# Kernel tuning notes

Hardware: AMD Instinct MI355X
Metric: run time of the kernel (lower is better)

## Reference

```python
import jax, jax.numpy as jnp
import numpy as np

B, N = 16, 286
EMB_DIM = 4
CLOUD_DIM = 4
NB = 3          # number_of_basis
HID = 150       # radial MLP hidden width
RADIUS = 3.0    # neighbor radius / max_radius of cosine basis
FF = 512


def sp5(x):
    # torch Softplus(beta=5)
    return jax.nn.softplus(5.0 * x) / 5.0


def cosine_basis(r):
    # e3nn CosineBasisModel embedding: cos^2 bumps on [0, RADIUS]
    centers = jnp.linspace(0.0, RADIUS, NB)
    step = centers[1] - centers[0]
    d = (r[..., None] - centers) / step                     # [B,N,N,NB]
    return jnp.cos(jnp.pi / 2 * d) ** 2 * (jnp.abs(d) < 1.0)


def cloud_conv(feats, dist, mask, ws, bs, dim_out):
    # radial MLP on pairwise distances -> per-pair [dim_out, dim_in] kernel (l=0 only)
    x = cosine_basis(dist)
    for w, b in zip(ws[:-1], bs[:-1]):
        x = sp5(x @ w + b)
    R = x @ ws[-1] + bs[-1]                                 # [B,N,N,dim_out*dim_in]
    b_, n_ = dist.shape[0], dist.shape[1]
    k = R.reshape(b_, n_, n_, dim_out, -1) * mask[..., None, None]
    nb = jnp.maximum(mask.sum(-1), 1.0)                     # neighbors per atom [B,N]
    out = jnp.einsum('zabij,zbj->zai', k, feats) / jnp.sqrt(nb)[..., None]
    return out


def setup_inputs() -> dict:
    key = jax.random.key(0)
    ks = jax.random.split(key, 32)
    xyz = jax.random.normal(ks[0], (B, N, 3), dtype=jnp.float32)
    Z = jax.random.randint(ks[1], (B, N), 0, 11)
    emb = jax.random.normal(ks[2], (11, EMB_DIM), dtype=jnp.float32)
    inp = {'xyz': xyz, 'Z': Z, 'emb': emb}
    # radial MLPs per cloud: 3 -> 150 -> 150 -> 150 -> dim_out*dim_in (=16)
    dims = [NB, HID, HID, HID, CLOUD_DIM * CLOUD_DIM]
    ki = 3
    for c in range(2):
        for l in range(4):
            w = jax.random.normal(ks[ki], (dims[l], dims[l + 1]), dtype=jnp.float32) / np.sqrt(dims[l])
            b = jnp.zeros((dims[l + 1],), dtype=jnp.float32)
            inp[f'c{c}_w{l}'] = w
            inp[f'c{c}_b{l}'] = b
            ki += 1
    cloud_out = CLOUD_DIM * 2  # cloud_dim * cloud_order^2 * nclouds = 8
    inp['fc_w'] = jax.random.normal(ks[ki], (cloud_out, FF), dtype=jnp.float32) / np.sqrt(cloud_out); ki += 1
    inp['fc_b'] = jnp.zeros((FF,), dtype=jnp.float32)
    inp['bn_g'] = jnp.ones((FF,), dtype=jnp.float32)
    inp['bn_b'] = jnp.zeros((FF,), dtype=jnp.float32)
    inp['out_w'] = jax.random.normal(ks[ki], (FF, 1), dtype=jnp.float32) / np.sqrt(FF); ki += 1
    inp['out_b'] = jnp.zeros((1,), dtype=jnp.float32)
    return inp


def reference(xyz, Z, emb,
              c0_w0, c0_b0, c0_w1, c0_b1, c0_w2, c0_b2, c0_w3, c0_b3,
              c1_w0, c1_b0, c1_w1, c1_b1, c1_w2, c1_b2, c1_w3, c1_b3,
              fc_w, fc_b, bn_g, bn_b, out_w, out_b):
    feats = emb[Z]                                          # [B,N,emb_dim]
    diff = xyz[:, :, None, :] - xyz[:, None, :, :]
    dist = jnp.sqrt(jnp.sum(diff * diff, -1) + 1e-12)       # [B,N,N]
    mask = (dist < RADIUS).astype(feats.dtype)
    f1 = cloud_conv(feats, dist, mask,
                    [c0_w0, c0_w1, c0_w2, c0_w3], [c0_b0, c0_b1, c0_b2, c0_b3], CLOUD_DIM)
    f2 = cloud_conv(f1, dist, mask,
                    [c1_w0, c1_w1, c1_w2, c1_w3], [c1_b0, c1_b1, c1_b2, c1_b3], CLOUD_DIM)
    feats_cat = jnp.concatenate([f1, f2], axis=2)           # [B,N,8]
    # lp_pool2d(norm=2, kernel=(N,1)) == L2 norm over atom dim
    pooled = jnp.sqrt(jnp.sum(feats_cat ** 2, axis=1))      # [B,8]
    h = jax.nn.softplus(pooled @ fc_w + fc_b)
    mean = h.mean(0)
    var = h.var(0)
    h = jax.nn.softplus((h - mean) / jnp.sqrt(var + 1e-5) * bn_g + bn_b)
    return jax.nn.sigmoid(h @ out_w + out_b)[:, 0]          # [B]
```

## Files before the change

### kernel.cpp

```cpp
#include <hip/hip_runtime.h>
#include <hip/hip_bf16.h>
#include <hip/hip_fp16.h>
#include <math.h>

#define B_SZ   16
#define N_ATOM 286
#define NT     1024
#define HIDW   150
#define FF_DIM 512
#define WPAD   152
#define WROWS  151
#define BLK_PER_Z 72

__device__ __forceinline__ float softplus_f(float x) {
  return fmaxf(x, 0.0f) + log1pf(expf(-fabsf(x)));
}
__device__ __forceinline__ float sp5_f(float x) {
  float t = 5.0f * x;
  return (fmaxf(t, 0.0f) + log1pf(expf(-fabsf(t)))) * 0.2f;
}

__global__ __launch_bounds__(256) void prep_kernel(
    const float* __restrict__ w1a, const float* __restrict__ b1a,
    const float* __restrict__ w2a, const float* __restrict__ b2a,
    const float* __restrict__ w1c, const float* __restrict__ b1c,
    const float* __restrict__ w2c, const float* __restrict__ b2c,
    float* __restrict__ Wp) {
  const int m = blockIdx.y;
  const float* W  = (m == 0) ? w1a : (m == 1) ? w2a : (m == 2) ? w1c : w2c;
  const float* Bb = (m == 0) ? b1a : (m == 1) ? b2a : (m == 2) ? b1c : b2c;
  int idx = blockIdx.x * 256 + threadIdx.x;
  if (idx < WROWS * WPAD) {
    int i = idx / WPAD, o = idx % WPAD;
    float v = 0.0f;
    if (o < HIDW) v = (i < HIDW) ? W[i * HIDW + o] : Bb[o];
    Wp[(size_t)m * WROWS * WPAD + idx] = v;
  }
}

__global__ __launch_bounds__(256) void table_kernel(
    const float* __restrict__ a_w0, const float* __restrict__ a_b0,
    const float* __restrict__ a_w3, const float* __restrict__ a_b3,
    const float* __restrict__ c_w0, const float* __restrict__ c_b0,
    const float* __restrict__ c_w3, const float* __restrict__ c_b3,
    const float* __restrict__ Wp,
    __half* __restrict__ tabh0, __half* __restrict__ tabh1) {
  __shared__ float actA[WPAD * 8];
  __shared__ float actB[WPAD * 8];

  const int nblk = NT / 8;
  const int cloud = (blockIdx.x >= nblk) ? 1 : 0;
  const int blk   = blockIdx.x - cloud * nblk;
  const float* w0 = cloud ? c_w0 : a_w0;  const float* b0 = cloud ? c_b0 : a_b0;
  const float* w3 = cloud ? c_w3 : a_w3;  const float* b3 = cloud ? c_b3 : a_b3;
  const float* __restrict__ Wp1 = Wp + (size_t)(cloud * 2)     * WROWS * WPAD;
  const float* __restrict__ Wp2 = Wp + (size_t)(cloud * 2 + 1) * WROWS * WPAD;
  __half* table = cloud ? tabh1 : tabh0;

  const int tid  = threadIdx.x;
  const int lane = tid & 63;
  const int wave = __builtin_amdgcn_readfirstlane(tid >> 6);
  const int e0   = wave * 2;
  const int gbase = blk * 8;
  const int jj = (lane < 38) ? lane : 37;

  float x0[3], x1[3];
  #pragma unroll
  for (int k = 0; k < 3; ++k) {
    float r0 = 3.0f * (float)(gbase + e0)     / (float)(NT - 1);
    float r1 = 3.0f * (float)(gbase + e0 + 1) / (float)(NT - 1);
    float d0 = (r0 - 1.5f * (float)k) * (1.0f / 1.5f);
    float d1 = (r1 - 1.5f * (float)k) * (1.0f / 1.5f);
    float c0 = cosf(1.57079632679489662f * d0);
    float c1 = cosf(1.57079632679489662f * d1);
    x0[k] = (fabsf(d0) < 1.0f) ? c0 * c0 : 0.0f;
    x1[k] = (fabsf(d1) < 1.0f) ? c1 * c1 : 0.0f;
  }

  #pragma unroll
  for (int c = 0; c < 3; ++c) {
    int o = lane + 64 * c;
    int oc = (o < HIDW) ? o : (HIDW - 1);
    float w00 = w0[oc], w01 = w0[HIDW + oc], w02 = w0[2 * HIDW + oc], bb = b0[oc];
    float h0 = sp5_f(bb + x0[0] * w00 + x0[1] * w01 + x0[2] * w02);
    float h1 = sp5_f(bb + x1[0] * w00 + x1[1] * w01 + x1[2] * w02);
    if (o < HIDW) *(float2*)(&actA[o * 8 + e0]) = make_float2(h0, h1);
  }

  {
    const float* __restrict__ Wb = Wp1 + 4 * jj;
    float4 a0 = *(const float4*)(Wp1 + HIDW * WPAD + 4 * jj);
    float4 a1 = a0;
    #pragma unroll 10
    for (int i = 0; i < HIDW; ++i) {
      float4 wv = *(const float4*)(Wb + i * WPAD);
      float2 h  = *(const float2*)(&actA[i * 8 + e0]);
      a0.x = __builtin_fmaf(h.x, wv.x, a0.x); a1.x = __builtin_fmaf(h.y, wv.x, a1.x);
      a0.y = __builtin_fmaf(h.x, wv.y, a0.y); a1.y = __builtin_fmaf(h.y, wv.y, a1.y);
      a0.z = __builtin_fmaf(h.x, wv.z, a0.z); a1.z = __builtin_fmaf(h.y, wv.z, a1.z);
      a0.w = __builtin_fmaf(h.x, wv.w, a0.w); a1.w = __builtin_fmaf(h.y, wv.w, a1.w);
    }
    *(float2*)(&actB[(4 * jj + 0) * 8 + e0]) = make_float2(sp5_f(a0.x), sp5_f(a1.x));
    *(float2*)(&actB[(4 * jj + 1) * 8 + e0]) = make_float2(sp5_f(a0.y), sp5_f(a1.y));
    *(float2*)(&actB[(4 * jj + 2) * 8 + e0]) = make_float2(sp5_f(a0.z), sp5_f(a1.z));
    *(float2*)(&actB[(4 * jj + 3) * 8 + e0]) = make_float2(sp5_f(a0.w), sp5_f(a1.w));
  }

  {
    const float* __restrict__ Wb = Wp2 + 4 * jj;
    float4 a0 = *(const float4*)(Wp2 + HIDW * WPAD + 4 * jj);
    float4 a1 = a0;
    #pragma unroll 10
    for (int i = 0; i < HIDW; ++i) {
      float4 wv = *(const float4*)(Wb + i * WPAD);
      float2 h  = *(const float2*)(&actB[i * 8 + e0]);
      a0.x = __builtin_fmaf(h.x, wv.x, a0.x); a1.x = __builtin_fmaf(h.y, wv.x, a1.x);
      a0.y = __builtin_fmaf(h.x, wv.y, a0.y); a1.y = __builtin_fmaf(h.y, wv.y, a1.y);
      a0.z = __builtin_fmaf(h.x, wv.z, a0.z); a1.z = __builtin_fmaf(h.y, wv.z, a1.z);
      a0.w = __builtin_fmaf(h.x, wv.w, a0.w); a1.w = __builtin_fmaf(h.y, wv.w, a1.w);
    }
    *(float2*)(&actA[(4 * jj + 0) * 8 + e0]) = make_float2(sp5_f(a0.x), sp5_f(a1.x));
    *(float2*)(&actA[(4 * jj + 1) * 8 + e0]) = make_float2(sp5_f(a0.y), sp5_f(a1.y));
    *(float2*)(&actA[(4 * jj + 2) * 8 + e0]) = make_float2(sp5_f(a0.z), sp5_f(a1.z));
    *(float2*)(&actA[(4 * jj + 3) * 8 + e0]) = make_float2(sp5_f(a0.w), sp5_f(a1.w));
  }

  {
    const int o  = lane & 15;
    const int ig = lane >> 4;
    float a0 = 0.f, a1 = 0.f;
    for (int i = ig; i < HIDW; i += 4) {
      float wv = w3[i * 16 + o];
      float h0 = actA[i * 8 + e0];
      float h1 = actA[i * 8 + e0 + 1];
      a0 = __builtin_fmaf(h0, wv, a0);
      a1 = __builtin_fmaf(h1, wv, a1);
    }
    a0 += __shfl_xor(a0, 16, 64); a0 += __shfl_xor(a0, 32, 64);
    a1 += __shfl_xor(a1, 16, 64); a1 += __shfl_xor(a1, 32, 64);
    if (lane < 16) {
      float bb = b3[o];
      table[(size_t)(gbase + e0)     * 16 + o] = __float2half(a0 + bb);
      table[(size_t)(gbase + e0 + 1) * 16 + o] = __float2half(a1 + bb);
    }
  }
}

__device__ __forceinline__ void cvt8(uint4 q, float* out) {
  const __half2* h = (const __half2*)&q;
  #pragma unroll
  for (int k = 0; k < 4; ++k) {
    float2 f = __half22float2(h[k]);
    out[2 * k] = f.x; out[2 * k + 1] = f.y;
  }
}

__global__ __launch_bounds__(256) void conv_kernel(
    const float* __restrict__ xyz, const int* __restrict__ Z,
    const float* __restrict__ emb, const float* __restrict__ feats_in,
    const __half* __restrict__ tabh, float* __restrict__ f_out, int gather) {
  __shared__ float xs[N_ATOM], ys[N_ATOM], zs[N_ATOM];
  __shared__ float fxs[N_ATOM], fys[N_ATOM], fzs[N_ATOM], fws[N_ATOM];
  const int tid  = threadIdx.x;
  const int wave = tid >> 6;
  const int lane = tid & 63;
  const int z = blockIdx.x / BLK_PER_Z;
  const int a = (blockIdx.x % BLK_PER_Z) * 4 + wave;

  for (int b = tid; b < N_ATOM; b += 256) {
    const float* p = xyz + ((size_t)z * N_ATOM + b) * 3;
    xs[b] = p[0]; ys[b] = p[1]; zs[b] = p[2];
    float4 fb;
    if (gather) {
      int zi = Z[z * N_ATOM + b];
      fb = *(const float4*)(emb + (size_t)zi * 4);
    } else {
      fb = *(const float4*)(feats_in + ((size_t)z * N_ATOM + b) * 4);
    }
    fxs[b] = fb.x; fys[b] = fb.y; fzs[b] = fb.z; fws[b] = fb.w;
  }
  __syncthreads();
  if (a >= N_ATOM) return;

  const float ax = xs[a], ay = ys[a], az = zs[a];

  float acc[4] = {0.f, 0.f, 0.f, 0.f};
  float cnt = 0.f;
  for (int b = lane; b < N_ATOM; b += 64) {
    float dx = ax - xs[b], dy = ay - ys[b], dz = az - zs[b];
    float r = sqrtf(dx * dx + dy * dy + dz * dz + 1e-12f);
    float msk = (r < 3.0f) ? 1.0f : 0.0f;
    float t = r * ((float)(NT - 1) / 3.0f);
    int idx = (int)t;
    if (idx > NT - 2) idx = NT - 2;
    float fr = t - (float)idx;
    const uint4* Tp = (const uint4*)(tabh + (size_t)idx * 16);
    uint4 q0 = Tp[0], q1 = Tp[1], q2 = Tp[2], q3 = Tp[3];
    float fbx = fxs[b], fby = fys[b], fbz = fzs[b], fbw = fws[b];
    cnt += msk;
    float r0[16], r1[16];
    cvt8(q0, r0); cvt8(q1, r0 + 8);
    cvt8(q2, r1); cvt8(q3, r1 + 8);
    #pragma unroll
    for (int i = 0; i < 4; ++i) {
      float v0 = r0[4 * i + 0] + fr * (r1[4 * i + 0] - r0[4 * i + 0]);
      float v1 = r0[4 * i + 1] + fr * (r1[4 * i + 1] - r0[4 * i + 1]);
      float v2 = r0[4 * i + 2] + fr * (r1[4 * i + 2] - r0[4 * i + 2]);
      float v3 = r0[4 * i + 3] + fr * (r1[4 * i + 3] - r0[4 * i + 3]);
      acc[i] = __builtin_fmaf(msk, v0 * fbx + v1 * fby + v2 * fbz + v3 * fbw,
                              acc[i]);
    }
  }
  #pragma unroll
  for (int m = 32; m > 0; m >>= 1) {
    #pragma unroll
    for (int i = 0; i < 4; ++i) acc[i] += __shfl_xor(acc[i], m, 64);
    cnt += __shfl_xor(cnt, m, 64);
  }
  if (lane == 0) {
    float nb = cnt < 1.0f ? 1.0f : cnt;
    float sc = 1.0f / sqrtf(nb);
    float4 o;
    o.x = acc[0] * sc; o.y = acc[1] * sc; o.z = acc[2] * sc; o.w = acc[3] * sc;
    *(float4*)(f_out + ((size_t)z * N_ATOM + a) * 4) = o;
  }
}

__global__ __launch_bounds__(256) void pool_kernel(
    const float* __restrict__ f1, const float* __restrict__ f2,
    float* __restrict__ pool_sq) {
  __shared__ float red[4][8];
  const int z = blockIdx.x;
  const int tid = threadIdx.x;
  const int lane = tid & 63, wave = tid >> 6;
  float s[8] = {0.f, 0.f, 0.f, 0.f, 0.f, 0.f, 0.f, 0.f};
  for (int a = tid; a < N_ATOM; a += 256) {
    float4 v1 = *(const float4*)(f1 + ((size_t)z * N_ATOM + a) * 4);
    float4 v2 = *(const float4*)(f2 + ((size_t)z * N_ATOM + a) * 4);
    s[0] += v1.x * v1.x; s[1] += v1.y * v1.y;
    s[2] += v1.z * v1.z; s[3] += v1.w * v1.w;
    s[4] += v2.x * v2.x; s[5] += v2.y * v2.y;
    s[6] += v2.z * v2.z; s[7] += v2.w * v2.w;
  }
  #pragma unroll
  for (int m = 32; m > 0; m >>= 1) {
    #pragma unroll
    for (int k = 0; k < 8; ++k) s[k] += __shfl_xor(s[k], m, 64);
  }
  if (lane == 0) {
    #pragma unroll
    for (int k = 0; k < 8; ++k) red[wave][k] = s[k];
  }
  __syncthreads();
  if (tid < 8)
    pool_sq[z * 8 + tid] = red[0][tid] + red[1][tid] + red[2][tid] + red[3][tid];
}

__global__ __launch_bounds__(512) void tail_kernel(
    const float* __restrict__ pool_sq,
    const float* __restrict__ fc_w, const float* __restrict__ fc_b,
    const float* __restrict__ bn_g, const float* __restrict__ bn_b,
    const float* __restrict__ out_w, const float* __restrict__ out_b,
    float* __restrict__ out) {
  __shared__ float pooled[16][8];
  __shared__ float part[8][16];
  const int tid = threadIdx.x;

  if (tid < 128) pooled[tid >> 3][tid & 7] = sqrtf(pool_sq[tid]);
  __syncthreads();

  const int f = tid;
  float hv[16];
  float mean = 0.f;
  #pragma unroll
  for (int z = 0; z < 16; ++z) {
    float a = fc_b[f];
    #pragma unroll
    for (int c = 0; c < 8; ++c) a += pooled[z][c] * fc_w[c * FF_DIM + f];
    hv[z] = softplus_f(a);
    mean += hv[z];
  }
  mean *= (1.0f / 16.0f);
  float var = 0.f;
  #pragma unroll
  for (int z = 0; z < 16; ++z) { float d = hv[z] - mean; var += d * d; }
  var *= (1.0f / 16.0f);
  float istd = 1.0f / sqrtf(var + 1e-5f);
  float g = bn_g[f], bb = bn_b[f], ow = out_w[f];
  float contrib[16];
  #pragma unroll
  for (int z = 0; z < 16; ++z)
    contrib[z] = softplus_f((hv[z] - mean) * istd * g + bb) * ow;

  const int lane = tid & 63, wv = tid >> 6;
  #pragma unroll
  for (int m = 32; m > 0; m >>= 1) {
    #pragma unroll
    for (int z = 0; z < 16; ++z) contrib[z] += __shfl_xor(contrib[z], m, 64);
  }
  if (lane == 0) {
    #pragma unroll
    for (int z = 0; z < 16; ++z) part[wv][z] = contrib[z];
  }
  __syncthreads();
  if (tid < 16) {
    float s = out_b[0];
    #pragma unroll
    for (int w8 = 0; w8 < 8; ++w8) s += part[w8][tid];
    out[tid] = 1.0f / (1.0f + expf(-s));
  }
}

extern "C" void kernel_launch(void* const* d_in, const int* in_sizes, int n_in,
                              void* d_out, int out_size, void* d_ws, size_t ws_size,
                              hipStream_t stream) {
  const float* xyz = (const float*)d_in[0];
  const int*   Z   = (const int*)d_in[1];
  const float* emb = (const float*)d_in[2];
  const float* c0[8]; const float* c1[8];
  for (int i = 0; i < 8; ++i) {
    c0[i] = (const float*)d_in[3 + i];
    c1[i] = (const float*)d_in[11 + i];
  }
  const float* fc_w  = (const float*)d_in[19];
  const float* fc_b  = (const float*)d_in[20];
  const float* bn_g  = (const float*)d_in[21];
  const float* bn_b  = (const float*)d_in[22];
  const float* out_w = (const float*)d_in[23];
  const float* out_b = (const float*)d_in[24];
  float* out = (float*)d_out;

  float* wsf = (float*)d_ws;
  float* Wp = wsf;
  float* f1 = Wp + (size_t)4 * WROWS * WPAD;
  float* f2 = f1 + (size_t)B_SZ * N_ATOM * 4;
  float* pool_sq = f2 + (size_t)B_SZ * N_ATOM * 4;
  __half* tabh0 = (__half*)(pool_sq + 128);
  __half* tabh1 = tabh0 + (size_t)NT * 16;

  {
    dim3 g((WROWS * WPAD + 255) / 256, 4);
    prep_kernel<<<g, 256, 0, stream>>>(c0[2], c0[3], c0[4], c0[5],
                                       c1[2], c1[3], c1[4], c1[5], Wp);
  }

  table_kernel<<<2 * (NT / 8), 256, 0, stream>>>(
      c0[0], c0[1], c0[6], c0[7],
      c1[0], c1[1], c1[6], c1[7],
      Wp, tabh0, tabh1);

  const int conv_blocks = B_SZ * BLK_PER_Z;
  conv_kernel<<<conv_blocks, 256, 0, stream>>>(xyz, Z, emb, (const float*)nullptr,
                                               tabh0, f1, 1);
  conv_kernel<<<conv_blocks, 256, 0, stream>>>(xyz, Z, emb, f1,
                                               tabh1, f2, 0);

  pool_kernel<<<B_SZ, 256, 0, stream>>>(f1, f2, pool_sq);

  tail_kernel<<<1, 512, 0, stream>>>(pool_sq, fc_w, fc_b, bn_g, bn_b,
                                     out_w, out_b, out);
}
```

Before: 180.1 us.

## Fuse all stages into one cooperative persistent kernel with grid-wide syncs

```diff
diff --git a/kernel.cpp b/kernel.cpp
--- a/kernel.cpp
+++ b/kernel.cpp
@@ -1,7 +1,9 @@
 #include <hip/hip_runtime.h>
-#include <hip/hip_bf16.h>
 #include <hip/hip_fp16.h>
+#include <hip/hip_cooperative_groups.h>
 #include <math.h>
+
+namespace cg = cooperative_groups;
 
 #define B_SZ   16
 #define N_ATOM 286
@@ -10,7 +12,6 @@
 #define FF_DIM 512
 #define WPAD   152
 #define WROWS  151
-#define BLK_PER_Z 72
 
 __device__ __forceinline__ float softplus_f(float x) {
   return fmaxf(x, 0.0f) + log1pf(expf(-fabsf(x)));
@@ -18,132 +19,6 @@
 __device__ __forceinline__ float sp5_f(float x) {
   float t = 5.0f * x;
   return (fmaxf(t, 0.0f) + log1pf(expf(-fabsf(t)))) * 0.2f;
-}
-
-__global__ __launch_bounds__(256) void prep_kernel(
-    const float* __restrict__ w1a, const float* __restrict__ b1a,
-    const float* __restrict__ w2a, const float* __restrict__ b2a,
-    const float* __restrict__ w1c, const float* __restrict__ b1c,
-    const float* __restrict__ w2c, const float* __restrict__ b2c,
-    float* __restrict__ Wp) {
-  const int m = blockIdx.y;
-  const float* W  = (m == 0) ? w1a : (m == 1) ? w2a : (m == 2) ? w1c : w2c;
-  const float* Bb = (m == 0) ? b1a : (m == 1) ? b2a : (m == 2) ? b1c : b2c;
-  int idx = blockIdx.x * 256 + threadIdx.x;
-  if (idx < WROWS * WPAD) {
-    int i = idx / WPAD, o = idx % WPAD;
-    float v = 0.0f;
-    if (o < HIDW) v = (i < HIDW) ? W[i * HIDW + o] : Bb[o];
-    Wp[(size_t)m * WROWS * WPAD + idx] = v;
-  }
-}
-
-__global__ __launch_bounds__(256) void table_kernel(
-    const float* __restrict__ a_w0, const float* __restrict__ a_b0,
-    const float* __restrict__ a_w3, const float* __restrict__ a_b3,
-    const float* __restrict__ c_w0, const float* __restrict__ c_b0,
-    const float* __restrict__ c_w3, const float* __restrict__ c_b3,
-    const float* __restrict__ Wp,
-    __half* __restrict__ tabh0, __half* __restrict__ tabh1) {
-  __shared__ float actA[WPAD * 8];
-  __shared__ float actB[WPAD * 8];
-
-  const int nblk = NT / 8;
-  const int cloud = (blockIdx.x >= nblk) ? 1 : 0;
-  const int blk   = blockIdx.x - cloud * nblk;
-  const float* w0 = cloud ? c_w0 : a_w0;  const float* b0 = cloud ? c_b0 : a_b0;
-  const float* w3 = cloud ? c_w3 : a_w3;  const float* b3 = cloud ? c_b3 : a_b3;
-  const float* __restrict__ Wp1 = Wp + (size_t)(cloud * 2)     * WROWS * WPAD;
-  const float* __restrict__ Wp2 = Wp + (size_t)(cloud * 2 + 1) * WROWS * WPAD;
-  __half* table = cloud ? tabh1 : tabh0;
-
-  const int tid  = threadIdx.x;
-  const int lane = tid & 63;
-  const int wave = __builtin_amdgcn_readfirstlane(tid >> 6);
-  const int e0   = wave * 2;
-  const int gbase = blk * 8;
-  const int jj = (lane < 38) ? lane : 37;
-
-  float x0[3], x1[3];
-  #pragma unroll
-  for (int k = 0; k < 3; ++k) {
-    float r0 = 3.0f * (float)(gbase + e0)     / (float)(NT - 1);
-    float r1 = 3.0f * (float)(gbase + e0 + 1) / (float)(NT - 1);
-    float d0 = (r0 - 1.5f * (float)k) * (1.0f / 1.5f);
-    float d1 = (r1 - 1.5f * (float)k) * (1.0f / 1.5f);
-    float c0 = cosf(1.57079632679489662f * d0);
-    float c1 = cosf(1.57079632679489662f * d1);
-    x0[k] = (fabsf(d0) < 1.0f) ? c0 * c0 : 0.0f;
-    x1[k] = (fabsf(d1) < 1.0f) ? c1 * c1 : 0.0f;
-  }
-
-  #pragma unroll
-  for (int c = 0; c < 3; ++c) {
-    int o = lane + 64 * c;
-    int oc = (o < HIDW) ? o : (HIDW - 1);
-    float w00 = w0[oc], w01 = w0[HIDW + oc], w02 = w0[2 * HIDW + oc], bb = b0[oc];
-    float h0 = sp5_f(bb + x0[0] * w00 + x0[1] * w01 + x0[2] * w02);
-    float h1 = sp5_f(bb + x1[0] * w00 + x1[1] * w01 + x1[2] * w02);
-    if (o < HIDW) *(float2*)(&actA[o * 8 + e0]) = make_float2(h0, h1);
-  }
-
-  {
-    const float* __restrict__ Wb = Wp1 + 4 * jj;
-    float4 a0 = *(const float4*)(Wp1 + HIDW * WPAD + 4 * jj);
-    float4 a1 = a0;
-    #pragma unroll 10
-    for (int i = 0; i < HIDW; ++i) {
-      float4 wv = *(const float4*)(Wb + i * WPAD);
-      float2 h  = *(const float2*)(&actA[i * 8 + e0]);
-      a0.x = __builtin_fmaf(h.x, wv.x, a0.x); a1.x = __builtin_fmaf(h.y, wv.x, a1.x);
-      a0.y = __builtin_fmaf(h.x, wv.y, a0.y); a1.y = __builtin_fmaf(h.y, wv.y, a1.y);
-      a0.z = __builtin_fmaf(h.x, wv.z, a0.z); a1.z = __builtin_fmaf(h.y, wv.z, a1.z);
-      a0.w = __builtin_fmaf(h.x, wv.w, a0.w); a1.w = __builtin_fmaf(h.y, wv.w, a1.w);
-    }
-    *(float2*)(&actB[(4 * jj + 0) * 8 + e0]) = make_float2(sp5_f(a0.x), sp5_f(a1.x));
-    *(float2*)(&actB[(4 * jj + 1) * 8 + e0]) = make_float2(sp5_f(a0.y), sp5_f(a1.y));
-    *(float2*)(&actB[(4 * jj + 2) * 8 + e0]) = make_float2(sp5_f(a0.z), sp5_f(a1.z));
-    *(float2*)(&actB[(4 * jj + 3) * 8 + e0]) = make_float2(sp5_f(a0.w), sp5_f(a1.w));
-  }
-
-  {
-    const float* __restrict__ Wb = Wp2 + 4 * jj;
-    float4 a0 = *(const float4*)(Wp2 + HIDW * WPAD + 4 * jj);
-    float4 a1 = a0;
-    #pragma unroll 10
-    for (int i = 0; i < HIDW; ++i) {
-      float4 wv = *(const float4*)(Wb + i * WPAD);
-      float2 h  = *(const float2*)(&actB[i * 8 + e0]);
-      a0.x = __builtin_fmaf(h.x, wv.x, a0.x); a1.x = __builtin_fmaf(h.y, wv.x, a1.x);
-      a0.y = __builtin_fmaf(h.x, wv.y, a0.y); a1.y = __builtin_fmaf(h.y, wv.y, a1.y);
-      a0.z = __builtin_fmaf(h.x, wv.z, a0.z); a1.z = __builtin_fmaf(h.y, wv.z, a1.z);
-      a0.w = __builtin_fmaf(h.x, wv.w, a0.w); a1.w = __builtin_fmaf(h.y, wv.w, a1.w);
-    }
-    *(float2*)(&actA[(4 * jj + 0) * 8 + e0]) = make_float2(sp5_f(a0.x), sp5_f(a1.x));
-    *(float2*)(&actA[(4 * jj + 1) * 8 + e0]) = make_float2(sp5_f(a0.y), sp5_f(a1.y));
-    *(float2*)(&actA[(4 * jj + 2) * 8 + e0]) = make_float2(sp5_f(a0.z), sp5_f(a1.z));
-    *(float2*)(&actA[(4 * jj + 3) * 8 + e0]) = make_float2(sp5_f(a0.w), sp5_f(a1.w));
-  }
-
-  {
-    const int o  = lane & 15;
-    const int ig = lane >> 4;
-    float a0 = 0.f, a1 = 0.f;
-    for (int i = ig; i < HIDW; i += 4) {
-      float wv = w3[i * 16 + o];
-      float h0 = actA[i * 8 + e0];
-      float h1 = actA[i * 8 + e0 + 1];
-      a0 = __builtin_fmaf(h0, wv, a0);
-      a1 = __builtin_fmaf(h1, wv, a1);
-    }
-    a0 += __shfl_xor(a0, 16, 64); a0 += __shfl_xor(a0, 32, 64);
-    a1 += __shfl_xor(a1, 16, 64); a1 += __shfl_xor(a1, 32, 64);
-    if (lane < 16) {
-      float bb = b3[o];
-      table[(size_t)(gbase + e0)     * 16 + o] = __float2half(a0 + bb);
-      table[(size_t)(gbase + e0 + 1) * 16 + o] = __float2half(a1 + bb);
-    }
-  }
 }
 
 __device__ __forceinline__ void cvt8(uint4 q, float* out) {
@@ -155,159 +30,283 @@
   }
 }
 
-__global__ __launch_bounds__(256) void conv_kernel(
+__global__ __launch_bounds__(256) void fused_kernel(
     const float* __restrict__ xyz, const int* __restrict__ Z,
-    const float* __restrict__ emb, const float* __restrict__ feats_in,
-    const __half* __restrict__ tabh, float* __restrict__ f_out, int gather) {
-  __shared__ float xs[N_ATOM], ys[N_ATOM], zs[N_ATOM];
-  __shared__ float fxs[N_ATOM], fys[N_ATOM], fzs[N_ATOM], fws[N_ATOM];
-  const int tid  = threadIdx.x;
-  const int wave = tid >> 6;
-  const int lane = tid & 63;
-  const int z = blockIdx.x / BLK_PER_Z;
-  const int a = (blockIdx.x % BLK_PER_Z) * 4 + wave;
-
-  for (int b = tid; b < N_ATOM; b += 256) {
-    const float* p = xyz + ((size_t)z * N_ATOM + b) * 3;
-    xs[b] = p[0]; ys[b] = p[1]; zs[b] = p[2];
-    float4 fb;
-    if (gather) {
-      int zi = Z[z * N_ATOM + b];
-      fb = *(const float4*)(emb + (size_t)zi * 4);
-    } else {
-      fb = *(const float4*)(feats_in + ((size_t)z * N_ATOM + b) * 4);
-    }
-    fxs[b] = fb.x; fys[b] = fb.y; fzs[b] = fb.z; fws[b] = fb.w;
-  }
-  __syncthreads();
-  if (a >= N_ATOM) return;
-
-  const float ax = xs[a], ay = ys[a], az = zs[a];
-
-  float acc[4] = {0.f, 0.f, 0.f, 0.f};
-  float cnt = 0.f;
-  for (int b = lane; b < N_ATOM; b += 64) {
-    float dx = ax - xs[b], dy = ay - ys[b], dz = az - zs[b];
-    float r = sqrtf(dx * dx + dy * dy + dz * dz + 1e-12f);
-    float msk = (r < 3.0f) ? 1.0f : 0.0f;
-    float t = r * ((float)(NT - 1) / 3.0f);
-    int idx = (int)t;
-    if (idx > NT - 2) idx = NT - 2;
-    float fr = t - (float)idx;
-    const uint4* Tp = (const uint4*)(tabh + (size_t)idx * 16);
-    uint4 q0 = Tp[0], q1 = Tp[1], q2 = Tp[2], q3 = Tp[3];
-    float fbx = fxs[b], fby = fys[b], fbz = fzs[b], fbw = fws[b];
-    cnt += msk;
-    float r0[16], r1[16];
-    cvt8(q0, r0); cvt8(q1, r0 + 8);
-    cvt8(q2, r1); cvt8(q3, r1 + 8);
-    #pragma unroll
-    for (int i = 0; i < 4; ++i) {
-      float v0 = r0[4 * i + 0] + fr * (r1[4 * i + 0] - r0[4 * i + 0]);
-      float v1 = r0[4 * i + 1] + fr * (r1[4 * i + 1] - r0[4 * i + 1]);
-      float v2 = r0[4 * i + 2] + fr * (r1[4 * i + 2] - r0[4 * i + 2]);
-      float v3 = r0[4 * i + 3] + fr * (r1[4 * i + 3] - r0[4 * i + 3]);
-      acc[i] = __builtin_fmaf(msk, v0 * fbx + v1 * fby + v2 * fbz + v3 * fbw,
-                              acc[i]);
-    }
-  }
-  #pragma unroll
-  for (int m = 32; m > 0; m >>= 1) {
-    #pragma unroll
-    for (int i = 0; i < 4; ++i) acc[i] += __shfl_xor(acc[i], m, 64);
-    cnt += __shfl_xor(cnt, m, 64);
-  }
-  if (lane == 0) {
-    float nb = cnt < 1.0f ? 1.0f : cnt;
-    float sc = 1.0f / sqrtf(nb);
-    float4 o;
-    o.x = acc[0] * sc; o.y = acc[1] * sc; o.z = acc[2] * sc; o.w = acc[3] * sc;
-    *(float4*)(f_out + ((size_t)z * N_ATOM + a) * 4) = o;
-  }
-}
-
-__global__ __launch_bounds__(256) void pool_kernel(
-    const float* __restrict__ f1, const float* __restrict__ f2,
-    float* __restrict__ pool_sq) {
-  __shared__ float red[4][8];
-  const int z = blockIdx.x;
-  const int tid = threadIdx.x;
-  const int lane = tid & 63, wave = tid >> 6;
-  float s[8] = {0.f, 0.f, 0.f, 0.f, 0.f, 0.f, 0.f, 0.f};
-  for (int a = tid; a < N_ATOM; a += 256) {
-    float4 v1 = *(const float4*)(f1 + ((size_t)z * N_ATOM + a) * 4);
-    float4 v2 = *(const float4*)(f2 + ((size_t)z * N_ATOM + a) * 4);
-    s[0] += v1.x * v1.x; s[1] += v1.y * v1.y;
-    s[2] += v1.z * v1.z; s[3] += v1.w * v1.w;
-    s[4] += v2.x * v2.x; s[5] += v2.y * v2.y;
-    s[6] += v2.z * v2.z; s[7] += v2.w * v2.w;
-  }
-  #pragma unroll
-  for (int m = 32; m > 0; m >>= 1) {
-    #pragma unroll
-    for (int k = 0; k < 8; ++k) s[k] += __shfl_xor(s[k], m, 64);
-  }
-  if (lane == 0) {
-    #pragma unroll
-    for (int k = 0; k < 8; ++k) red[wave][k] = s[k];
-  }
-  __syncthreads();
-  if (tid < 8)
-    pool_sq[z * 8 + tid] = red[0][tid] + red[1][tid] + red[2][tid] + red[3][tid];
-}
-
-__global__ __launch_bounds__(512) void tail_kernel(
-    const float* __restrict__ pool_sq,
+    const float* __restrict__ emb,
+    const float* __restrict__ a_w0, const float* __restrict__ a_b0,
+    const float* __restrict__ a_w1, const float* __restrict__ a_b1,
+    const float* __restrict__ a_w2, const float* __restrict__ a_b2,
+    const float* __restrict__ a_w3, const float* __restrict__ a_b3,
+    const float* __restrict__ c_w0, const float* __restrict__ c_b0,
+    const float* __restrict__ c_w1, const float* __restrict__ c_b1,
+    const float* __restrict__ c_w2, const float* __restrict__ c_b2,
+    const float* __restrict__ c_w3, const float* __restrict__ c_b3,
     const float* __restrict__ fc_w, const float* __restrict__ fc_b,
     const float* __restrict__ bn_g, const float* __restrict__ bn_b,
     const float* __restrict__ out_w, const float* __restrict__ out_b,
-    float* __restrict__ out) {
-  __shared__ float pooled[16][8];
-  __shared__ float part[8][16];
-  const int tid = threadIdx.x;
-
-  if (tid < 128) pooled[tid >> 3][tid & 7] = sqrtf(pool_sq[tid]);
-  __syncthreads();
-
-  const int f = tid;
-  float hv[16];
-  float mean = 0.f;
-  #pragma unroll
-  for (int z = 0; z < 16; ++z) {
-    float a = fc_b[f];
-    #pragma unroll
-    for (int c = 0; c < 8; ++c) a += pooled[z][c] * fc_w[c * FF_DIM + f];
-    hv[z] = softplus_f(a);
-    mean += hv[z];
-  }
-  mean *= (1.0f / 16.0f);
-  float var = 0.f;
-  #pragma unroll
-  for (int z = 0; z < 16; ++z) { float d = hv[z] - mean; var += d * d; }
-  var *= (1.0f / 16.0f);
-  float istd = 1.0f / sqrtf(var + 1e-5f);
-  float g = bn_g[f], bb = bn_b[f], ow = out_w[f];
-  float contrib[16];
-  #pragma unroll
-  for (int z = 0; z < 16; ++z)
-    contrib[z] = softplus_f((hv[z] - mean) * istd * g + bb) * ow;
-
-  const int lane = tid & 63, wv = tid >> 6;
-  #pragma unroll
-  for (int m = 32; m > 0; m >>= 1) {
-    #pragma unroll
-    for (int z = 0; z < 16; ++z) contrib[z] += __shfl_xor(contrib[z], m, 64);
-  }
-  if (lane == 0) {
-    #pragma unroll
-    for (int z = 0; z < 16; ++z) part[wv][z] = contrib[z];
-  }
-  __syncthreads();
-  if (tid < 16) {
-    float s = out_b[0];
-    #pragma unroll
-    for (int w8 = 0; w8 < 8; ++w8) s += part[w8][tid];
-    out[tid] = 1.0f / (1.0f + expf(-s));
+    float* __restrict__ out,
+    float* __restrict__ Wp, float* __restrict__ f1, float* __restrict__ f2,
+    float* __restrict__ pool_sq,
+    __half* __restrict__ tabh0, __half* __restrict__ tabh1) {
+  __shared__ float sA[WPAD * 8];
+  __shared__ float sB[WPAD * 8];
+
+  cg::grid_group grid = cg::this_grid();
+  const int tid  = threadIdx.x;
+  const int lane = tid & 63;
+  const int wave = __builtin_amdgcn_readfirstlane(tid >> 6);
+
+  {
+    const int total = 4 * WROWS * WPAD;
+    for (int idx = blockIdx.x * 256 + tid; idx < total; idx += 256 * 256) {
+      int m  = idx / (WROWS * WPAD);
+      int r2 = idx - m * (WROWS * WPAD);
+      int i = r2 / WPAD, o = r2 - i * WPAD;
+      const float* W  = (m == 0) ? a_w1 : (m == 1) ? a_w2 : (m == 2) ? c_w1 : c_w2;
+      const float* Bb = (m == 0) ? a_b1 : (m == 1) ? a_b2 : (m == 2) ? c_b1 : c_b2;
+      float v = 0.0f;
+      if (o < HIDW) v = (i < HIDW) ? W[i * HIDW + o] : Bb[o];
+      Wp[idx] = v;
+    }
+  }
+  grid.sync();
+
+  {
+    const int nblk = NT / 8;
+    const int cloud = (blockIdx.x >= nblk) ? 1 : 0;
+    const int blk   = blockIdx.x - cloud * nblk;
+    const float* w0 = cloud ? c_w0 : a_w0;  const float* b0 = cloud ? c_b0 : a_b0;
+    const float* w3 = cloud ? c_w3 : a_w3;  const float* b3 = cloud ? c_b3 : a_b3;
+    const float* __restrict__ Wp1 = Wp + (size_t)(cloud * 2)     * WROWS * WPAD;
+    const float* __restrict__ Wp2 = Wp + (size_t)(cloud * 2 + 1) * WROWS * WPAD;
+    __half* table = cloud ? tabh1 : tabh0;
+    const int e0 = wave * 2;
+    const int gbase = blk * 8;
+    const int jj = (lane < 38) ? lane : 37;
+
+    float x0[3], x1[3];
+    #pragma unroll
+    for (int k = 0; k < 3; ++k) {
+      float r0 = 3.0f * (float)(gbase + e0)     / (float)(NT - 1);
+      float r1 = 3.0f * (float)(gbase + e0 + 1) / (float)(NT - 1);
+      float d0 = (r0 - 1.5f * (float)k) * (1.0f / 1.5f);
+      float d1 = (r1 - 1.5f * (float)k) * (1.0f / 1.5f);
+      float cc0 = cosf(1.57079632679489662f * d0);
+      float cc1 = cosf(1.57079632679489662f * d1);
+      x0[k] = (fabsf(d0) < 1.0f) ? cc0 * cc0 : 0.0f;
+      x1[k] = (fabsf(d1) < 1.0f) ? cc1 * cc1 : 0.0f;
+    }
+
+    #pragma unroll
+    for (int c = 0; c < 3; ++c) {
+      int o = lane + 64 * c;
+      int oc = (o < HIDW) ? o : (HIDW - 1);
+      float w00 = w0[oc], w01 = w0[HIDW + oc], w02 = w0[2 * HIDW + oc], bb = b0[oc];
+      float h0 = sp5_f(bb + x0[0] * w00 + x0[1] * w01 + x0[2] * w02);
+      float h1 = sp5_f(bb + x1[0] * w00 + x1[1] * w01 + x1[2] * w02);
+      if (o < HIDW) *(float2*)(&sA[o * 8 + e0]) = make_float2(h0, h1);
+    }
+
+    {
+      const float* __restrict__ Wb = Wp1 + 4 * jj;
+      float4 a0 = *(const float4*)(Wp1 + HIDW * WPAD + 4 * jj);
+      float4 a1 = a0;
+      #pragma unroll 10
+      for (int i = 0; i < HIDW; ++i) {
+        float4 wv = *(const float4*)(Wb + i * WPAD);
+        float2 h  = *(const float2*)(&sA[i * 8 + e0]);
+        a0.x = __builtin_fmaf(h.x, wv.x, a0.x); a1.x = __builtin_fmaf(h.y, wv.x, a1.x);
+        a0.y = __builtin_fmaf(h.x, wv.y, a0.y); a1.y = __builtin_fmaf(h.y, wv.y, a1.y);
+        a0.z = __builtin_fmaf(h.x, wv.z, a0.z); a1.z = __builtin_fmaf(h.y, wv.z, a1.z);
+        a0.w = __builtin_fmaf(h.x, wv.w, a0.w); a1.w = __builtin_fmaf(h.y, wv.w, a1.w);
+      }
+      *(float2*)(&sB[(4 * jj + 0) * 8 + e0]) = make_float2(sp5_f(a0.x), sp5_f(a1.x));
+      *(float2*)(&sB[(4 * jj + 1) * 8 + e0]) = make_float2(sp5_f(a0.y), sp5_f(a1.y));
+      *(float2*)(&sB[(4 * jj + 2) * 8 + e0]) = make_float2(sp5_f(a0.z), sp5_f(a1.z));
+      *(float2*)(&sB[(4 * jj + 3) * 8 + e0]) = make_float2(sp5_f(a0.w), sp5_f(a1.w));
+    }
+    {
+      const float* __restrict__ Wb = Wp2 + 4 * jj;
+      float4 a0 = *(const float4*)(Wp2 + HIDW * WPAD + 4 * jj);
+      float4 a1 = a0;
+      #pragma unroll 10
+      for (int i = 0; i < HIDW; ++i) {
+        float4 wv = *(const float4*)(Wb + i * WPAD);
+        float2 h  = *(const float2*)(&sB[i * 8 + e0]);
+        a0.x = __builtin_fmaf(h.x, wv.x, a0.x); a1.x = __builtin_fmaf(h.y, wv.x, a1.x);
+        a0.y = __builtin_fmaf(h.x, wv.y, a0.y); a1.y = __builtin_fmaf(h.y, wv.y, a1.y);
+        a0.z = __builtin_fmaf(h.x, wv.z, a0.z); a1.z = __builtin_fmaf(h.y, wv.z, a1.z);
+        a0.w = __builtin_fmaf(h.x, wv.w, a0.w); a1.w = __builtin_fmaf(h.y, wv.w, a1.w);
+      }
+      *(float2*)(&sA[(4 * jj + 0) * 8 + e0]) = make_float2(sp5_f(a0.x), sp5_f(a1.x));
+      *(float2*)(&sA[(4 * jj + 1) * 8 + e0]) = make_float2(sp5_f(a0.y), sp5_f(a1.y));
+      *(float2*)(&sA[(4 * jj + 2) * 8 + e0]) = make_float2(sp5_f(a0.z), sp5_f(a1.z));
+      *(float2*)(&sA[(4 * jj + 3) * 8 + e0]) = make_float2(sp5_f(a0.w), sp5_f(a1.w));
+    }
+    {
+      const int o  = lane & 15;
+      const int ig = lane >> 4;
+      float a0 = 0.f, a1 = 0.f;
+      for (int i = ig; i < HIDW; i += 4) {
+        float wv = w3[i * 16 + o];
+        float h0 = sA[i * 8 + e0];
+        float h1 = sA[i * 8 + e0 + 1];
+        a0 = __builtin_fmaf(h0, wv, a0);
+        a1 = __builtin_fmaf(h1, wv, a1);
+      }
+      a0 += __shfl_xor(a0, 16, 64); a0 += __shfl_xor(a0, 32, 64);
+      a1 += __shfl_xor(a1, 16, 64); a1 += __shfl_xor(a1, 32, 64);
+      if (lane < 16) {
+        float bb = b3[o];
+        table[(size_t)(gbase + e0)     * 16 + o] = __float2half(a0 + bb);
+        table[(size_t)(gbase + e0 + 1) * 16 + o] = __float2half(a1 + bb);
+      }
+    }
+  }
+  grid.sync();
+
+  {
+    const int z   = blockIdx.x >> 4;
+    const int sub = blockIdx.x & 15;
+    const int a0r = sub * 18;
+    const int a1r = (a0r + 18 < N_ATOM) ? a0r + 18 : N_ATOM;
+
+    for (int pass = 0; pass < 2; ++pass) {
+      const __half* __restrict__ tabh = pass ? tabh1 : tabh0;
+      float* __restrict__ fout = pass ? f2 : f1;
+
+      for (int b = tid; b < N_ATOM; b += 256) {
+        const float* p = xyz + ((size_t)z * N_ATOM + b) * 3;
+        sA[b] = p[0]; sA[304 + b] = p[1]; sA[608 + b] = p[2];
+        float4 fb;
+        if (pass == 0) {
+          int zi = Z[z * N_ATOM + b];
+          fb = *(const float4*)(emb + (size_t)zi * 4);
+        } else {
+          fb = *(const float4*)(f1 + ((size_t)z * N_ATOM + b) * 4);
+        }
+        sB[b] = fb.x; sB[304 + b] = fb.y; sB[608 + b] = fb.z; sB[912 + b] = fb.w;
+      }
+      __syncthreads();
+
+      for (int row = a0r + wave; row < a1r; row += 4) {
+        const float ax = sA[row], ay = sA[304 + row], az = sA[608 + row];
+        float acc[4] = {0.f, 0.f, 0.f, 0.f};
+        float cnt = 0.f;
+        for (int b = lane; b < N_ATOM; b += 64) {
+          float dx = ax - sA[b], dy = ay - sA[304 + b], dz = az - sA[608 + b];
+          float r = sqrtf(dx * dx + dy * dy + dz * dz + 1e-12f);
+          float msk = (r < 3.0f) ? 1.0f : 0.0f;
+          float t = r * ((float)(NT - 1) / 3.0f);
+          int idx = (int)t;
+          if (idx > NT - 2) idx = NT - 2;
+          float fr = t - (float)idx;
+          const uint4* Tp = (const uint4*)(tabh + (size_t)idx * 16);
+          uint4 q0 = Tp[0], q1 = Tp[1], q2 = Tp[2], q3 = Tp[3];
+          float fbx = sB[b], fby = sB[304 + b], fbz = sB[608 + b], fbw = sB[912 + b];
+          cnt += msk;
+          float r0[16], r1[16];
+          cvt8(q0, r0); cvt8(q1, r0 + 8);
+          cvt8(q2, r1); cvt8(q3, r1 + 8);
+          #pragma unroll
+          for (int i = 0; i < 4; ++i) {
+            float v0 = r0[4 * i + 0] + fr * (r1[4 * i + 0] - r0[4 * i + 0]);
+            float v1 = r0[4 * i + 1] + fr * (r1[4 * i + 1] - r0[4 * i + 1]);
+            float v2 = r0[4 * i + 2] + fr * (r1[4 * i + 2] - r0[4 * i + 2]);
+            float v3 = r0[4 * i + 3] + fr * (r1[4 * i + 3] - r0[4 * i + 3]);
+            acc[i] = __builtin_fmaf(msk, v0 * fbx + v1 * fby + v2 * fbz + v3 * fbw,
+                                    acc[i]);
+          }
+        }
+        #pragma unroll
+        for (int m = 32; m > 0; m >>= 1) {
+          #pragma unroll
+          for (int i = 0; i < 4; ++i) acc[i] += __shfl_xor(acc[i], m, 64);
+          cnt += __shfl_xor(cnt, m, 64);
+        }
+        if (lane == 0) {
+          float nb = cnt < 1.0f ? 1.0f : cnt;
+          float sc = 1.0f / sqrtf(nb);
+          float4 o;
+          o.x = acc[0] * sc; o.y = acc[1] * sc; o.z = acc[2] * sc; o.w = acc[3] * sc;
+          *(float4*)(fout + ((size_t)z * N_ATOM + row) * 4) = o;
+        }
+      }
+      grid.sync();
+    }
+  }
+
+  if (blockIdx.x < B_SZ) {
+    const int z = blockIdx.x;
+    float s[8] = {0.f, 0.f, 0.f, 0.f, 0.f, 0.f, 0.f, 0.f};
+    for (int a = tid; a < N_ATOM; a += 256) {
+      float4 v1 = *(const float4*)(f1 + ((size_t)z * N_ATOM + a) * 4);
+      float4 v2 = *(const float4*)(f2 + ((size_t)z * N_ATOM + a) * 4);
+      s[0] += v1.x * v1.x; s[1] += v1.y * v1.y;
+      s[2] += v1.z * v1.z; s[3] += v1.w * v1.w;
+      s[4] += v2.x * v2.x; s[5] += v2.y * v2.y;
+      s[6] += v2.z * v2.z; s[7] += v2.w * v2.w;
+    }
+    #pragma unroll
+    for (int m = 32; m > 0; m >>= 1) {
+      #pragma unroll
+      for (int k = 0; k < 8; ++k) s[k] += __shfl_xor(s[k], m, 64);
+    }
+    if (lane == 0) {
+      #pragma unroll
+      for (int k = 0; k < 8; ++k) sB[wave * 8 + k] = s[k];
+    }
+    __syncthreads();
+    if (tid < 8)
+      pool_sq[z * 8 + tid] = sB[tid] + sB[8 + tid] + sB[16 + tid] + sB[24 + tid];
+  }
+  grid.sync();
+
+  if (blockIdx.x == 0) {
+    if (tid < 128) sA[tid] = sqrtf(pool_sq[tid]);
+    __syncthreads();
+    float acc16[16];
+    #pragma unroll
+    for (int zz = 0; zz < 16; ++zz) acc16[zz] = 0.f;
+    #pragma unroll
+    for (int ff = 0; ff < 2; ++ff) {
+      const int f = tid + ff * 256;
+      float hv[16];
+      float mean = 0.f;
+      #pragma unroll
+      for (int zz = 0; zz < 16; ++zz) {
+        float a = fc_b[f];
+        #pragma unroll
+        for (int c = 0; c < 8; ++c) a += sA[zz * 8 + c] * fc_w[c * FF_DIM + f];
+        hv[zz] = softplus_f(a);
+        mean += hv[zz];
+      }
+      mean *= (1.0f / 16.0f);
+      float var = 0.f;
+      #pragma unroll
+      for (int zz = 0; zz < 16; ++zz) { float d = hv[zz] - mean; var += d * d; }
+      var *= (1.0f / 16.0f);
+      float istd = 1.0f / sqrtf(var + 1e-5f);
+      float g = bn_g[f], bb = bn_b[f], ow = out_w[f];
+      #pragma unroll
+      for (int zz = 0; zz < 16; ++zz)
+        acc16[zz] += softplus_f((hv[zz] - mean) * istd * g + bb) * ow;
+    }
+    #pragma unroll
+    for (int m = 32; m > 0; m >>= 1) {
+      #pragma unroll
+      for (int zz = 0; zz < 16; ++zz) acc16[zz] += __shfl_xor(acc16[zz], m, 64);
+    }
+    if (lane == 0) {
+      #pragma unroll
+      for (int zz = 0; zz < 16; ++zz) sA[128 + wave * 16 + zz] = acc16[zz];
+    }
+    __syncthreads();
+    if (tid < 16) {
+      float s = out_b[0] + sA[128 + tid] + sA[144 + tid] + sA[160 + tid]
+                         + sA[176 + tid];
+      out[tid] = 1.0f / (1.0f + expf(-s));
+    }
   }
 }
 
@@ -317,11 +316,14 @@
   const float* xyz = (const float*)d_in[0];
   const int*   Z   = (const int*)d_in[1];
   const float* emb = (const float*)d_in[2];
-  const float* c0[8]; const float* c1[8];
-  for (int i = 0; i < 8; ++i) {
-    c0[i] = (const float*)d_in[3 + i];
-    c1[i] = (const float*)d_in[11 + i];
-  }
+  const float* a_w0 = (const float*)d_in[3];  const float* a_b0 = (const float*)d_in[4];
+  const float* a_w1 = (const float*)d_in[5];  const float* a_b1 = (const float*)d_in[6];
+  const float* a_w2 = (const float*)d_in[7];  const float* a_b2 = (const float*)d_in[8];
+  const float* a_w3 = (const float*)d_in[9];  const float* a_b3 = (const float*)d_in[10];
+  const float* c_w0 = (const float*)d_in[11]; const float* c_b0 = (const float*)d_in[12];
+  const float* c_w1 = (const float*)d_in[13]; const float* c_b1 = (const float*)d_in[14];
+  const float* c_w2 = (const float*)d_in[15]; const float* c_b2 = (const float*)d_in[16];
+  const float* c_w3 = (const float*)d_in[17]; const float* c_b3 = (const float*)d_in[18];
   const float* fc_w  = (const float*)d_in[19];
   const float* fc_b  = (const float*)d_in[20];
   const float* bn_g  = (const float*)d_in[21];
@@ -338,25 +340,17 @@
   __half* tabh0 = (__half*)(pool_sq + 128);
   __half* tabh1 = tabh0 + (size_t)NT * 16;
 
-  {
-    dim3 g((WROWS * WPAD + 255) / 256, 4);
-    prep_kernel<<<g, 256, 0, stream>>>(c0[2], c0[3], c0[4], c0[5],
-                                       c1[2], c1[3], c1[4], c1[5], Wp);
-  }
-
-  table_kernel<<<2 * (NT / 8), 256, 0, stream>>>(
-      c0[0], c0[1], c0[6], c0[7],
-      c1[0], c1[1], c1[6], c1[7],
-      Wp, tabh0, tabh1);
-
-  const int conv_blocks = B_SZ * BLK_PER_Z;
-  conv_kernel<<<conv_blocks, 256, 0, stream>>>(xyz, Z, emb, (const float*)nullptr,
-                                               tabh0, f1, 1);
-  conv_kernel<<<conv_blocks, 256, 0, stream>>>(xyz, Z, emb, f1,
-                                               tabh1, f2, 0);
-
-  pool_kernel<<<B_SZ, 256, 0, stream>>>(f1, f2, pool_sq);
-
-  tail_kernel<<<1, 512, 0, stream>>>(pool_sq, fc_w, fc_b, bn_g, bn_b,
-                                     out_w, out_b, out);
-}
+  void* params[] = {
+    (void*)&xyz, (void*)&Z, (void*)&emb,
+    (void*)&a_w0, (void*)&a_b0, (void*)&a_w1, (void*)&a_b1,
+    (void*)&a_w2, (void*)&a_b2, (void*)&a_w3, (void*)&a_b3,
+    (void*)&c_w0, (void*)&c_b0, (void*)&c_w1, (void*)&c_b1,
+    (void*)&c_w2, (void*)&c_b2, (void*)&c_w3, (void*)&c_b3,
+    (void*)&fc_w, (void*)&fc_b, (void*)&bn_g, (void*)&bn_b,
+    (void*)&out_w, (void*)&out_b, (void*)&out,
+    (void*)&Wp, (void*)&f1, (void*)&f2, (void*)&pool_sq,
+    (void*)&tabh0, (void*)&tabh1
+  };
+  hipLaunchCooperativeKernel((void*)fused_kernel, dim3(256), dim3(256),
+                             params, 0, stream);
+}
```

After: 359.0 us. 99.3% more time.
